# Kernel optimization log

Measured on AMD Instinct MI355X. Metric: run time of the kernel, lower is better.

The kernel has to match this reference:

```python
import jax, jax.numpy as jnp
import numpy as np

WS, SHIFT, NH, DIM = 8, 4, 4, 128
HD = DIM // NH
B, H, W = 16, 128, 128
N = WS * WS
LOG100 = float(np.log(100.0))


def _rel_tables():
    r = np.arange(-(WS - 1), WS, dtype=np.float32)
    tab = np.stack(np.meshgrid(r, r, indexing='ij'), axis=-1) / (WS - 1) * 8.0
    tab = np.sign(tab) * np.log2(np.abs(tab) + 1.0) / np.log2(8.0)
    coords = np.stack(np.meshgrid(np.arange(WS), np.arange(WS), indexing='ij')).reshape(2, -1)
    rel = (coords[:, :, None] - coords[:, None, :]).transpose(1, 2, 0).copy()
    rel[:, :, 0] += WS - 1
    rel[:, :, 1] += WS - 1
    rel[:, :, 0] *= 2 * WS - 1
    return jnp.asarray(tab.reshape(-1, 2)), jnp.asarray(rel.sum(-1))

REL_TABLE, REL_INDEX = _rel_tables()  # ((2WS-1)^2, 2), (N, N)


def _attn_mask():
    img = np.zeros((H, W), np.float32)
    cnt = 0
    for hs in (slice(0, -WS), slice(-WS, -SHIFT), slice(-SHIFT, None)):
        for ws in (slice(0, -WS), slice(-WS, -SHIFT), slice(-SHIFT, None)):
            img[hs, ws] = cnt
            cnt += 1
    mw = img.reshape(H // WS, WS, W // WS, WS).transpose(0, 2, 1, 3).reshape(-1, N)
    d = mw[:, None, :] - mw[:, :, None]
    return jnp.asarray(np.where(d != 0, -100.0, 0.0).astype(np.float32))

ATTN_MASK = _attn_mask()  # (nW, N, N)


def _ln(x, w, b, eps=1e-5):
    mu = x.mean(-1, keepdims=True)
    var = ((x - mu) ** 2).mean(-1, keepdims=True)
    return (x - mu) * jax.lax.rsqrt(var + eps) * w + b


def setup_inputs() -> dict:
    key = jax.random.key(0)
    ks = jax.random.split(key, 8)
    s = 0.02
    return {
        'x': jax.random.normal(ks[0], (B, DIM, H, W), jnp.float32),
        'norm1_w': jnp.ones((DIM,), jnp.float32),
        'norm1_b': jnp.zeros((DIM,), jnp.float32),
        'qkv_w': jax.random.normal(ks[1], (3 * DIM, DIM), jnp.float32) * s,
        'q_bias': jnp.zeros((DIM,), jnp.float32),
        'v_bias': jnp.zeros((DIM,), jnp.float32),
        'logit_scale': jnp.full((NH, 1, 1), float(np.log(10.0)), jnp.float32),
        'cpb_w1': jax.random.normal(ks[2], (512, 2), jnp.float32) * s,
        'cpb_b1': jnp.zeros((512,), jnp.float32),
        'cpb_w2': jax.random.normal(ks[3], (NH, 512), jnp.float32) * s,
        'proj_w': jax.random.normal(ks[4], (DIM, DIM), jnp.float32) * s,
        'proj_b': jnp.zeros((DIM,), jnp.float32),
        'norm2_w': jnp.ones((DIM,), jnp.float32),
        'norm2_b': jnp.zeros((DIM,), jnp.float32),
        'fc1_w': jax.random.normal(ks[5], (4 * DIM, DIM), jnp.float32) * s,
        'fc1_b': jnp.zeros((4 * DIM,), jnp.float32),
        'fc2_w': jax.random.normal(ks[6], (DIM, 4 * DIM), jnp.float32) * s,
        'fc2_b': jnp.zeros((DIM,), jnp.float32),
    }


def reference(x, norm1_w, norm1_b, qkv_w, q_bias, v_bias, logit_scale,
              cpb_w1, cpb_b1, cpb_w2, proj_w, proj_b,
              norm2_w, norm2_b, fc1_w, fc1_b, fc2_w, fc2_b):
    xb = jnp.transpose(x, (0, 2, 3, 1))                 # (B,H,W,C)
    shortcut = xb.reshape(B, H * W, DIM)
    shifted = jnp.roll(xb, (-SHIFT, -SHIFT), axis=(1, 2))
    # window partition -> (B*nW, N, C)
    xw = shifted.reshape(B, H // WS, WS, W // WS, WS, DIM)
    xw = xw.transpose(0, 1, 3, 2, 4, 5).reshape(-1, N, DIM)
    B_ = xw.shape[0]
    qkv_bias = jnp.concatenate([q_bias, jnp.zeros_like(v_bias), v_bias])
    qkv = xw @ qkv_w.T + qkv_bias
    qkv = qkv.reshape(B_, N, 3, NH, HD).transpose(2, 0, 3, 1, 4)
    q, k, v = qkv[0], qkv[1], qkv[2]                    # (B_,NH,N,HD)
    qn = q / jnp.maximum(jnp.linalg.norm(q, axis=-1, keepdims=True), 1e-12)
    kn = k / jnp.maximum(jnp.linalg.norm(k, axis=-1, keepdims=True), 1e-12)
    attn = jnp.einsum('bhnd,bhmd->bhnm', qn, kn)
    attn = attn * jnp.exp(jnp.minimum(logit_scale, LOG100))
    # continuous relative position bias: tiny MLP over log-spaced coords + gather
    tab = jax.nn.relu(REL_TABLE @ cpb_w1.T + cpb_b1) @ cpb_w2.T    # ((2WS-1)^2, NH)
    bias = tab[REL_INDEX.reshape(-1)].reshape(N, N, NH).transpose(2, 0, 1)
    attn = attn + (16.0 * jax.nn.sigmoid(bias))[None]
    nW = ATTN_MASK.shape[0]
    attn = attn.reshape(B_ // nW, nW, NH, N, N) + ATTN_MASK[None, :, None]
    attn = jax.nn.softmax(attn.reshape(B_, NH, N, N), axis=-1)
    out = jnp.einsum('bhnm,bhmd->bhnd', attn, v).transpose(0, 2, 1, 3).reshape(B_, N, DIM)
    out = out @ proj_w.T + proj_b
    # window reverse + reverse cyclic shift
    out = out.reshape(B, H // WS, W // WS, WS, WS, DIM).transpose(0, 1, 3, 2, 4, 5).reshape(B, H, W, DIM)
    out = jnp.roll(out, (SHIFT, SHIFT), axis=(1, 2)).reshape(B, H * W, DIM)
    x1 = shortcut + _ln(out, norm1_w, norm1_b)          # Swin-v2 post-norm residual
    hdn = jax.nn.silu(x1 @ fc1_w.T + fc1_b) @ fc2_w.T + fc2_b
    x2 = x1 + _ln(hdn, norm2_w, norm2_b)
    return x2.reshape(B, H, W, DIM).transpose(0, 3, 1, 2)
```

## Files before the change

kernel.cpp:

```cpp
#include <hip/hip_runtime.h>
#include <cstdint>
#include <cstddef>

typedef __bf16 bf16;
typedef __bf16 bf16x8 __attribute__((ext_vector_type(8)));
typedef float f32x4 __attribute__((ext_vector_type(4)));

#define MFMA16(a, b, c) __builtin_amdgcn_mfma_f32_16x16x32_bf16((a), (b), (c), 0, 0, 0)

__device__ __forceinline__ float bf2f(bf16 v) { return (float)v; }

#define OFF_SCALES 65536
#define OFF_FLAG   65552
#define OFF_QKVB   65600
#define OFF_PROJB  67136
#define OFF_N1W    67648
#define OFF_N1B    68160
#define OFF_FC1B   68672
#define OFF_FC2B   70720
#define OFF_N2W    71232
#define OFF_N2B    71744
#define OFF_QKVW   73728
#define OFF_PROJW  172032
#define OFF_FC1W   204800
#define OFF_FC2W   335872
#define OFF_X1BUF  524288

template<int DT>
__device__ __forceinline__ void g_ld4(const void* base, size_t idx, float* o) {
    if constexpr (DT == 0) {
        uint2 d = *(const uint2*)((const bf16*)base + idx);
        const bf16* p = (const bf16*)&d;
        o[0] = bf2f(p[0]); o[1] = bf2f(p[1]); o[2] = bf2f(p[2]); o[3] = bf2f(p[3]);
    } else {
        float4 d = *(const float4*)((const float*)base + idx);
        o[0] = d.x; o[1] = d.y; o[2] = d.z; o[3] = d.w;
    }
}

__global__ void k_precompute(const void* __restrict__ cpb_w1, const void* __restrict__ cpb_b1,
                             const void* __restrict__ cpb_w2, const void* __restrict__ logit_scale,
                             const void* __restrict__ qkv_w_raw,
                             float* __restrict__ biasAll, float* __restrict__ scales,
                             int* __restrict__ flag)
{
    __shared__ float w1s[1024];
    __shared__ float b1s[512];
    __shared__ float w2s[2048];
    __shared__ float tabv[225][4];
    __shared__ int s_cnt;
    const int t = threadIdx.x;
    if (t == 0) s_cnt = 0;
    __syncthreads();
    {
        const unsigned short* u = (const unsigned short*)qkv_w_raw;
        int c = 0;
        for (int i = t; i < 1024; i += 256) {
            const int e = (u[i] >> 7) & 0xFF;
            if (e >= 0x90 || (e != 0 && e <= 0x60)) ++c;
        }
        atomicAdd(&s_cnt, c);
    }
    __syncthreads();
    const int isf = (s_cnt > 64) ? 1 : 0;
    if (t == 0) *flag = isf;
    if (isf) {
        const float* w1 = (const float*)cpb_w1;
        const float* b1 = (const float*)cpb_b1;
        const float* w2 = (const float*)cpb_w2;
        for (int i = t; i < 1024; i += 256) w1s[i] = w1[i];
        for (int i = t; i < 512;  i += 256) b1s[i] = b1[i];
        for (int i = t; i < 2048; i += 256) w2s[i] = w2[i];
        if (t < 4) scales[t] = expf(fminf(((const float*)logit_scale)[t], 4.6051701859880914f));
    } else {
        const bf16* w1 = (const bf16*)cpb_w1;
        const bf16* b1 = (const bf16*)cpb_b1;
        const bf16* w2 = (const bf16*)cpb_w2;
        for (int i = t; i < 1024; i += 256) w1s[i] = bf2f(w1[i]);
        for (int i = t; i < 512;  i += 256) b1s[i] = bf2f(b1[i]);
        for (int i = t; i < 2048; i += 256) w2s[i] = bf2f(w2[i]);
        if (t < 4) scales[t] = expf(fminf(bf2f(((const bf16*)logit_scale)[t]), 4.6051701859880914f));
    }
    __syncthreads();
    if (t < 225) {
        const int i = t / 15, j = t % 15;
        auto relf = [](int tt) -> float {
            float tf = (float)tt * (8.0f / 7.0f);
            float a = log2f(fabsf(tf) + 1.0f) * (1.0f / 3.0f);
            return tt < 0 ? -a : a;
        };
        const float x0 = relf(i - 7), x1 = relf(j - 7);
        float a0 = 0.f, a1 = 0.f, a2 = 0.f, a3 = 0.f;
        for (int jj = 0; jj < 512; ++jj) {
            float hv = w1s[jj*2] * x0 + w1s[jj*2+1] * x1 + b1s[jj];
            hv = fmaxf(hv, 0.0f);
            a0 += w2s[jj]        * hv;
            a1 += w2s[512 + jj]  * hv;
            a2 += w2s[1024 + jj] * hv;
            a3 += w2s[1536 + jj] * hv;
        }
        tabv[t][0] = a0; tabv[t][1] = a1; tabv[t][2] = a2; tabv[t][3] = a3;
    }
    __syncthreads();
    for (int idx = t; idx < 4*64*64; idx += 256) {
        const int h = idx >> 12, rem = idx & 4095, i = rem >> 6, j = rem & 63;
        const int di = (i >> 3) - (j >> 3) + 7;
        const int dj = (i & 7) - (j & 7) + 7;
        const float bv = tabv[di*15 + dj][h];
        biasAll[idx] = 16.0f / (1.0f + expf(-bv));
    }
}

__global__ void k_convert(
    const void* __restrict__ qkv_w, const void* __restrict__ proj_w,
    const void* __restrict__ fc1w, const void* __restrict__ fc2w,
    const void* __restrict__ q_bias, const void* __restrict__ v_bias,
    const void* __restrict__ proj_b, const void* __restrict__ n1w, const void* __restrict__ n1b,
    const void* __restrict__ fc1b, const void* __restrict__ fc2b,
    const void* __restrict__ n2w, const void* __restrict__ n2b,
    const int* __restrict__ flag, char* __restrict__ ws)
{
    const int isf = *flag;
    const int g  = blockIdx.x * 256 + threadIdx.x;
    const int gs = gridDim.x * 256;
    bf16* qw = (bf16*)(ws + OFF_QKVW);
    bf16* pw = (bf16*)(ws + OFF_PROJW);
    bf16* f1 = (bf16*)(ws + OFF_FC1W);
    bf16* f2 = (bf16*)(ws + OFF_FC2W);
    if (isf) {
        const float* a = (const float*)qkv_w;  for (int i = g; i < 49152; i += gs) qw[i] = (bf16)a[i];
        const float* b = (const float*)proj_w; for (int i = g; i < 16384; i += gs) pw[i] = (bf16)b[i];
        const float* c = (const float*)fc1w;   for (int i = g; i < 65536; i += gs) f1[i] = (bf16)c[i];
        const float* d = (const float*)fc2w;   for (int i = g; i < 65536; i += gs) f2[i] = (bf16)d[i];
    } else {
        const bf16* a = (const bf16*)qkv_w;  for (int i = g; i < 49152; i += gs) qw[i] = a[i];
        const bf16* b = (const bf16*)proj_w; for (int i = g; i < 16384; i += gs) pw[i] = b[i];
        const bf16* c = (const bf16*)fc1w;   for (int i = g; i < 65536; i += gs) f1[i] = c[i];
        const bf16* d = (const bf16*)fc2w;   for (int i = g; i < 65536; i += gs) f2[i] = d[i];
    }
    auto ldf = [&](const void* p, int i) -> float {
        return isf ? ((const float*)p)[i] : bf2f(((const bf16*)p)[i]);
    };
    float* qb  = (float*)(ws + OFF_QKVB);
    float* pb  = (float*)(ws + OFF_PROJB);
    float* w1  = (float*)(ws + OFF_N1W);
    float* b1  = (float*)(ws + OFF_N1B);
    float* f1b = (float*)(ws + OFF_FC1B);
    float* f2b = (float*)(ws + OFF_FC2B);
    float* w2  = (float*)(ws + OFF_N2W);
    float* b2  = (float*)(ws + OFF_N2B);
    for (int i = g; i < 384; i += gs)
        qb[i] = (i < 128) ? ldf(q_bias, i) : ((i < 256) ? 0.0f : ldf(v_bias, i - 256));
    for (int i = g; i < 512; i += gs) f1b[i] = ldf(fc1b, i);
    for (int i = g; i < 128; i += gs) {
        pb[i]  = ldf(proj_b, i); w1[i] = ldf(n1w, i); b1[i] = ldf(n1b, i);
        f2b[i] = ldf(fc2b, i);   w2[i] = ldf(n2w, i); b2[i] = ldf(n2b, i);
    }
}

template<int DT>
__global__ __launch_bounds__(256, 2) void k_attn(
    const void* __restrict__ x,
    const bf16* __restrict__ qkvw, const float* __restrict__ qkvb,
    const bf16* __restrict__ projw, const float* __restrict__ projb,
    const float* __restrict__ n1wf, const float* __restrict__ n1bf,
    const float* __restrict__ biasAll, const float* __restrict__ scales,
    const int* __restrict__ flag, bf16* __restrict__ x1out)
{
    if (*flag != DT) return;

    __shared__ __align__(16) char smem[75008];
    bf16* Xs    = (bf16*)smem;
    bf16* qkvs  = (bf16*)(smem + 17408);
    bf16* Ps    = qkvs;
    bf16* x1s   = qkvs;
    bf16* vs    = (bf16*)(smem + 54272);
    bf16* Os    = vs;
    float* invqs = (float*)(smem + 72704);
    float* invks = (float*)(smem + 73728);
    int*   rid   = (int*)(smem + 74752);

    const int tid  = threadIdx.x;
    const int wv   = tid >> 6;
    const int lane = tid & 63;
    const int l15  = lane & 15;
    const int quad = lane >> 4;

    const int bid = blockIdx.x;
    const int b   = bid >> 8;
    const int wh  = (bid >> 4) & 15;
    const int ww  = bid & 15;

    {
        const int c  = tid & 127;
        const int rb = tid >> 7;
        const int w0 = ww*8 + 4;
        const int w1 = (ww*8 + 8) & 127;
#pragma unroll
        for (int k = 0; k < 4; ++k) {
            const int r    = k*2 + rb;
            const int srch = (wh*8 + r + 4) & 127;
            const size_t rowbase = (((size_t)(b*128 + c))*128 + srch)*128;
            float va[4], vb[4];
            g_ld4<DT>(x, rowbase + w0, va);
            g_ld4<DT>(x, rowbase + w1, vb);
#pragma unroll
            for (int j = 0; j < 4; ++j) {
                Xs[(r*8 + j)*136 + c]     = (bf16)va[j];
                Xs[(r*8 + 4 + j)*136 + c] = (bf16)vb[j];
            }
        }
        if (tid < 64) {
            const int rr = tid >> 3, cc = tid & 7;
            const int hs = wh*8 + rr, wsc = ww*8 + cc;
            const int rh = (hs  < 120) ? 0 : ((hs  < 124) ? 1 : 2);
            const int rw = (wsc < 120) ? 0 : ((wsc < 124) ? 1 : 2);
            rid[tid] = rh*3 + rw;
        }
    }
    __syncthreads();

    {
        f32x4 acc[4][6];
#pragma unroll
        for (int mt = 0; mt < 4; ++mt)
#pragma unroll
            for (int nl = 0; nl < 6; ++nl) acc[mt][nl] = (f32x4){0.f, 0.f, 0.f, 0.f};
#pragma unroll
        for (int ks = 0; ks < 4; ++ks) {
            bf16x8 a[4];
#pragma unroll
            for (int mt = 0; mt < 4; ++mt)
                a[mt] = *(const bf16x8*)&Xs[(mt*16 + l15)*136 + ks*32 + quad*8];
#pragma unroll
            for (int nl = 0; nl < 6; ++nl) {
                const int o = (wv*6 + nl)*16 + l15;
                bf16x8 bw = *(const bf16x8*)&qkvw[(size_t)o*128 + ks*32 + quad*8];
#pragma unroll
                for (int mt = 0; mt < 4; ++mt)
                    acc[mt][nl] = MFMA16(a[mt], bw, acc[mt][nl]);
            }
        }
#pragma unroll
        for (int nl = 0; nl < 6; ++nl) {
            const int col = (wv*6 + nl)*16 + l15;
            const float bias = qkvb[col];
#pragma unroll
            for (int mt = 0; mt < 4; ++mt)
#pragma unroll
                for (int r = 0; r < 4; ++r) {
                    const int row = mt*16 + quad*4 + r;
                    const float v = acc[mt][nl][r] + bias;
                    if (col < 256) qkvs[row*264 + col] = (bf16)v;
                    else           vs[(col - 256)*72 + row] = (bf16)v;
                }
        }
    }
    __syncthreads();

    {
        const int n = lane;
        const bf16* qrow = &qkvs[n*264 + wv*32];
        const bf16* krow = &qkvs[n*264 + 128 + wv*32];
        float sq = 0.f, sk = 0.f;
#pragma unroll
        for (int dd = 0; dd < 4; ++dd) {
            bf16x8 vq = *(const bf16x8*)(qrow + dd*8);
            bf16x8 vk = *(const bf16x8*)(krow + dd*8);
#pragma unroll
            for (int e = 0; e < 8; ++e) {
                const float fq = (float)vq[e]; sq += fq*fq;
                const float fk = (float)vk[e]; sk += fk*fk;
            }
        }
        invqs[wv*64 + n] = 1.0f / fmaxf(sqrtf(sq), 1e-12f);
        invks[wv*64 + n] = 1.0f / fmaxf(sqrtf(sk), 1e-12f);
    }
    __syncthreads();

    {
        const float scale = scales[wv];
        f32x4 s[4][4];
#pragma unroll
        for (int mt = 0; mt < 4; ++mt)
#pragma unroll
            for (int nt = 0; nt < 4; ++nt) s[mt][nt] = (f32x4){0.f, 0.f, 0.f, 0.f};
        bf16x8 aq[4];
#pragma unroll
        for (int mt = 0; mt < 4; ++mt)
            aq[mt] = *(const bf16x8*)&qkvs[(mt*16 + l15)*264 + wv*32 + quad*8];
#pragma unroll
        for (int nt = 0; nt < 4; ++nt) {
            bf16x8 bk = *(const bf16x8*)&qkvs[(nt*16 + l15)*264 + 128 + wv*32 + quad*8];
#pragma unroll
            for (int mt = 0; mt < 4; ++mt)
                s[mt][nt] = MFMA16(aq[mt], bk, s[mt][nt]);
        }
        __syncthreads();
        const float* bg = biasAll + wv*4096;
        const bool bnd = (wh == 15) || (ww == 15);
        float ikj[4]; int rj[4];
#pragma unroll
        for (int nt = 0; nt < 4; ++nt) {
            ikj[nt] = invks[wv*64 + nt*16 + l15];
            rj[nt]  = rid[nt*16 + l15];
        }
#pragma unroll
        for (int mt = 0; mt < 4; ++mt)
#pragma unroll
            for (int r = 0; r < 4; ++r) {
                const int i = mt*16 + quad*4 + r;
                const float iqs = invqs[wv*64 + i] * scale;
                const int ri = rid[i];
#pragma unroll
                for (int nt = 0; nt < 4; ++nt) {
                    const int j = nt*16 + l15;
                    float v = s[mt][nt][r] * (iqs * ikj[nt]) + bg[i*64 + j];
                    if (bnd && (ri != rj[nt])) v -= 100.0f;
                    s[mt][nt][r] = v;
                }
            }
#pragma unroll
        for (int mt = 0; mt < 4; ++mt) {
            float mx[4], sm[4];
#pragma unroll
            for (int r = 0; r < 4; ++r) {
                float m = fmaxf(fmaxf(s[mt][0][r], s[mt][1][r]), fmaxf(s[mt][2][r], s[mt][3][r]));
                m = fmaxf(m, __shfl_xor(m, 1));
                m = fmaxf(m, __shfl_xor(m, 2));
                m = fmaxf(m, __shfl_xor(m, 4));
                m = fmaxf(m, __shfl_xor(m, 8));
                mx[r] = m; sm[r] = 0.f;
            }
#pragma unroll
            for (int nt = 0; nt < 4; ++nt)
#pragma unroll
                for (int r = 0; r < 4; ++r) {
                    const float e = __expf(s[mt][nt][r] - mx[r]);
                    s[mt][nt][r] = e;
                    sm[r] += e;
                }
#pragma unroll
            for (int r = 0; r < 4; ++r) {
                float t2 = sm[r];
                t2 += __shfl_xor(t2, 1);
                t2 += __shfl_xor(t2, 2);
                t2 += __shfl_xor(t2, 4);
                t2 += __shfl_xor(t2, 8);
                sm[r] = 1.0f / t2;
            }
#pragma unroll
            for (int nt = 0; nt < 4; ++nt)
#pragma unroll
                for (int r = 0; r < 4; ++r) {
                    const float p = s[mt][nt][r] * sm[r];
                    Ps[wv*64*72 + (mt*16 + quad*4 + r)*72 + nt*16 + l15] = (bf16)p;
                }
        }
    }
    __syncthreads();

    {
        f32x4 o[4][2];
#pragma unroll
        for (int mt = 0; mt < 4; ++mt)
#pragma unroll
            for (int nt = 0; nt < 2; ++nt) o[mt][nt] = (f32x4){0.f, 0.f, 0.f, 0.f};
#pragma unroll
        for (int ks = 0; ks < 2; ++ks) {
            bf16x8 ap[4];
#pragma unroll
            for (int mt = 0; mt < 4; ++mt)
                ap[mt] = *(const bf16x8*)&Ps[wv*64*72 + (mt*16 + l15)*72 + ks*32 + quad*8];
#pragma unroll
            for (int nt = 0; nt < 2; ++nt) {
                bf16x8 bv = *(const bf16x8*)&vs[(wv*32 + nt*16 + l15)*72 + ks*32 + quad*8];
#pragma unroll
                for (int mt = 0; mt < 4; ++mt)
                    o[mt][nt] = MFMA16(ap[mt], bv, o[mt][nt]);
            }
        }
        __syncthreads();
#pragma unroll
        for (int mt = 0; mt < 4; ++mt)
#pragma unroll
            for (int nt = 0; nt < 2; ++nt)
#pragma unroll
                for (int r = 0; r < 4; ++r) {
                    const int i = mt*16 + quad*4 + r;
                    Os[i*136 + wv*32 + nt*16 + l15] = (bf16)o[mt][nt][r];
                }
    }
    __syncthreads();

    {
        f32x4 pa[4][2];
#pragma unroll
        for (int mt = 0; mt < 4; ++mt)
#pragma unroll
            for (int nt = 0; nt < 2; ++nt) pa[mt][nt] = (f32x4){0.f, 0.f, 0.f, 0.f};
#pragma unroll
        for (int ks = 0; ks < 4; ++ks) {
            bf16x8 ao[4];
#pragma unroll
            for (int mt = 0; mt < 4; ++mt)
                ao[mt] = *(const bf16x8*)&Os[(mt*16 + l15)*136 + ks*32 + quad*8];
#pragma unroll
            for (int nt = 0; nt < 2; ++nt) {
                const int oc = wv*32 + nt*16 + l15;
                bf16x8 bw = *(const bf16x8*)&projw[(size_t)oc*128 + ks*32 + quad*8];
#pragma unroll
                for (int mt = 0; mt < 4; ++mt)
                    pa[mt][nt] = MFMA16(ao[mt], bw, pa[mt][nt]);
            }
        }
        float pb[2], wn[2], bn[2];
#pragma unroll
        for (int nt = 0; nt < 2; ++nt) {
            const int oc = wv*32 + nt*16 + l15;
            pb[nt] = projb[oc]; wn[nt] = n1wf[oc]; bn[nt] = n1bf[oc];
        }
        float* ps = invqs;
        float* pq = invks;
#pragma unroll
        for (int mt = 0; mt < 4; ++mt)
#pragma unroll
            for (int r = 0; r < 4; ++r) {
                pa[mt][0][r] += pb[0];
                pa[mt][1][r] += pb[1];
                float sv = pa[mt][0][r] + pa[mt][1][r];
                sv += __shfl_xor(sv, 1); sv += __shfl_xor(sv, 2);
                sv += __shfl_xor(sv, 4); sv += __shfl_xor(sv, 8);
                if (l15 == 0) ps[wv*64 + mt*16 + quad*4 + r] = sv;
            }
        __syncthreads();
        float mu[4][4];
#pragma unroll
        for (int mt = 0; mt < 4; ++mt)
#pragma unroll
            for (int r = 0; r < 4; ++r) {
                const int i = mt*16 + quad*4 + r;
                mu[mt][r] = (ps[i] + ps[64+i] + ps[128+i] + ps[192+i]) * (1.0f/128.0f);
                const float d0 = pa[mt][0][r] - mu[mt][r];
                const float d1 = pa[mt][1][r] - mu[mt][r];
                float sv = d0*d0 + d1*d1;
                sv += __shfl_xor(sv, 1); sv += __shfl_xor(sv, 2);
                sv += __shfl_xor(sv, 4); sv += __shfl_xor(sv, 8);
                if (l15 == 0) pq[wv*64 + i] = sv;
            }
        __syncthreads();
#pragma unroll
        for (int mt = 0; mt < 4; ++mt)
#pragma unroll
            for (int r = 0; r < 4; ++r) {
                const int i = mt*16 + quad*4 + r;
                const float var = (pq[i] + pq[64+i] + pq[128+i] + pq[192+i]) * (1.0f/128.0f);
                const float rstd = rsqrtf(var + 1e-5f);
#pragma unroll
                for (int nt = 0; nt < 2; ++nt) {
                    const int oc = wv*32 + nt*16 + l15;
                    const float y = (pa[mt][nt][r] - mu[mt][r]) * rstd * wn[nt] + bn[nt];
                    const float x1v = bf2f(Xs[i*136 + oc]) + y;
                    x1s[i*136 + oc] = (bf16)x1v;
                }
            }
    }
    __syncthreads();

    {
        const int n = tid >> 2, part = tid & 3;
        const int rr = n >> 3, cc = n & 7;
        const int hf = (wh*8 + rr + 4) & 127;
        const int wf = (ww*8 + cc + 4) & 127;
        bf16* dst = x1out + ((size_t)b*16384 + hf*128 + wf)*128 + part*32;
        const uint4* srcq = (const uint4*)&x1s[n*136 + part*32];
#pragma unroll
        for (int k2 = 0; k2 < 4; ++k2)
            ((uint4*)dst)[k2] = srcq[k2];
    }
}

template<int DT>
__global__ __launch_bounds__(256, 4) void k_mlp(
    const bf16* __restrict__ x1, const bf16* __restrict__ fc1w, const float* __restrict__ fc1bf,
    const bf16* __restrict__ fc2w, const float* __restrict__ fc2bf,
    const float* __restrict__ n2wf, const float* __restrict__ n2bf,
    const int* __restrict__ flag, void* __restrict__ out)
{
    if (*flag != DT) return;

    __shared__ __align__(16) bf16 x1s[64*136];
    __shared__ __align__(16) bf16 hs[64*136];
    __shared__ float ps[256];
    __shared__ float pq[256];

    const int tid  = threadIdx.x;
    const int wv   = tid >> 6;
    const int lane = tid & 63;
    const int l15  = lane & 15;
    const int quad = lane >> 4;
    const int bid  = blockIdx.x;

    {
        const int n = tid >> 2, part = tid & 3;
        const uint4* src = (const uint4*)(x1 + ((size_t)bid*64 + n)*128 + part*32);
        uint4* dst = (uint4*)&x1s[n*136 + part*32];
#pragma unroll
        for (int k = 0; k < 4; ++k) dst[k] = src[k];
    }
    __syncthreads();

    f32x4 ya[4][2];
#pragma unroll
    for (int mt = 0; mt < 4; ++mt)
#pragma unroll
        for (int nt = 0; nt < 2; ++nt) ya[mt][nt] = (f32x4){0.f, 0.f, 0.f, 0.f};

#pragma unroll
    for (int ch = 0; ch < 4; ++ch) {
        if (ch) __syncthreads();
        f32x4 ha[4][2];
#pragma unroll
        for (int mt = 0; mt < 4; ++mt)
#pragma unroll
            for (int nt = 0; nt < 2; ++nt) ha[mt][nt] = (f32x4){0.f, 0.f, 0.f, 0.f};
#pragma unroll
        for (int ks = 0; ks < 4; ++ks) {
            bf16x8 a[4];
#pragma unroll
            for (int mt = 0; mt < 4; ++mt)
                a[mt] = *(const bf16x8*)&x1s[(mt*16 + l15)*136 + ks*32 + quad*8];
#pragma unroll
            for (int nt = 0; nt < 2; ++nt) {
                const int hid = ch*128 + wv*32 + nt*16 + l15;
                bf16x8 bw = *(const bf16x8*)&fc1w[(size_t)hid*128 + ks*32 + quad*8];
#pragma unroll
                for (int mt = 0; mt < 4; ++mt)
                    ha[mt][nt] = MFMA16(a[mt], bw, ha[mt][nt]);
            }
        }
#pragma unroll
        for (int nt = 0; nt < 2; ++nt) {
            const int hid = ch*128 + wv*32 + nt*16 + l15;
            const float bb = fc1bf[hid];
            const int hl = wv*32 + nt*16 + l15;
#pragma unroll
            for (int mt = 0; mt < 4; ++mt)
#pragma unroll
                for (int r = 0; r < 4; ++r) {
                    float v = ha[mt][nt][r] + bb;
                    v = v / (1.0f + __expf(-v));
                    hs[(mt*16 + quad*4 + r)*136 + hl] = (bf16)v;
                }
        }
        __syncthreads();
#pragma unroll
        for (int ks = 0; ks < 4; ++ks) {
            bf16x8 ah[4];
#pragma unroll
            for (int mt = 0; mt < 4; ++mt)
                ah[mt] = *(const bf16x8*)&hs[(mt*16 + l15)*136 + ks*32 + quad*8];
#pragma unroll
            for (int nt = 0; nt < 2; ++nt) {
                const int oc = wv*32 + nt*16 + l15;
                bf16x8 bw = *(const bf16x8*)&fc2w[(size_t)oc*512 + ch*128 + ks*32 + quad*8];
#pragma unroll
                for (int mt = 0; mt < 4; ++mt)
                    ya[mt][nt] = MFMA16(ah[mt], bw, ya[mt][nt]);
            }
        }
    }
    __syncthreads();

    {
        float pb[2], wn[2], bn[2];
#pragma unroll
        for (int nt = 0; nt < 2; ++nt) {
            const int oc = wv*32 + nt*16 + l15;
            pb[nt] = fc2bf[oc]; wn[nt] = n2wf[oc]; bn[nt] = n2bf[oc];
        }
#pragma unroll
        for (int mt = 0; mt < 4; ++mt)
#pragma unroll
            for (int r = 0; r < 4; ++r) {
                ya[mt][0][r] += pb[0];
                ya[mt][1][r] += pb[1];
                float sv = ya[mt][0][r] + ya[mt][1][r];
                sv += __shfl_xor(sv, 1); sv += __shfl_xor(sv, 2);
                sv += __shfl_xor(sv, 4); sv += __shfl_xor(sv, 8);
                if (l15 == 0) ps[wv*64 + mt*16 + quad*4 + r] = sv;
            }
        __syncthreads();
        float mu[4][4];
#pragma unroll
        for (int mt = 0; mt < 4; ++mt)
#pragma unroll
            for (int r = 0; r < 4; ++r) {
                const int i = mt*16 + quad*4 + r;
                mu[mt][r] = (ps[i] + ps[64+i] + ps[128+i] + ps[192+i]) * (1.0f/128.0f);
                const float d0 = ya[mt][0][r] - mu[mt][r];
                const float d1 = ya[mt][1][r] - mu[mt][r];
                float sv = d0*d0 + d1*d1;
                sv += __shfl_xor(sv, 1); sv += __shfl_xor(sv, 2);
                sv += __shfl_xor(sv, 4); sv += __shfl_xor(sv, 8);
                if (l15 == 0) pq[wv*64 + i] = sv;
            }
        __syncthreads();
        bf16* x2s = hs;
#pragma unroll
        for (int mt = 0; mt < 4; ++mt)
#pragma unroll
            for (int r = 0; r < 4; ++r) {
                const int i = mt*16 + quad*4 + r;
                const float var = (pq[i] + pq[64+i] + pq[128+i] + pq[192+i]) * (1.0f/128.0f);
                const float rstd = rsqrtf(var + 1e-5f);
#pragma unroll
                for (int nt = 0; nt < 2; ++nt) {
                    const int oc = wv*32 + nt*16 + l15;
                    const float yv = (ya[mt][nt][r] - mu[mt][r]) * rstd * wn[nt] + bn[nt];
                    const float x2v = bf2f(x1s[i*136 + oc]) + yv;
                    x2s[i*136 + oc] = (bf16)x2v;
                }
            }
    }
    __syncthreads();

    {
        const int c = tid >> 1, half = tid & 1;
        const int b = bid >> 8, rem = bid & 255;
        const int hh = rem >> 1, w0 = (rem & 1)*64;
        const bf16* x2s = hs;
        const size_t base_off = ((size_t)(b*128 + c))*16384 + hh*128 + w0 + half*32;
        if constexpr (DT == 0) {
            const unsigned short* x2u = (const unsigned short*)hs;
            bf16* dst = (bf16*)out + base_off;
#pragma unroll
            for (int g = 0; g < 4; ++g) {
                const int tb = half*32 + g*8;
                uint4 u;
                u.x = (unsigned)x2u[(tb+0)*136 + c] | ((unsigned)x2u[(tb+1)*136 + c] << 16);
                u.y = (unsigned)x2u[(tb+2)*136 + c] | ((unsigned)x2u[(tb+3)*136 + c] << 16);
                u.z = (unsigned)x2u[(tb+4)*136 + c] | ((unsigned)x2u[(tb+5)*136 + c] << 16);
                u.w = (unsigned)x2u[(tb+6)*136 + c] | ((unsigned)x2u[(tb+7)*136 + c] << 16);
                ((uint4*)dst)[g] = u;
            }
        } else {
            float* dst = (float*)out + base_off;
#pragma unroll
            for (int g = 0; g < 4; ++g) {
                const int tb = half*32 + g*8;
                float4 u0, u1;
                u0.x = bf2f(x2s[(tb+0)*136 + c]); u0.y = bf2f(x2s[(tb+1)*136 + c]);
                u0.z = bf2f(x2s[(tb+2)*136 + c]); u0.w = bf2f(x2s[(tb+3)*136 + c]);
                u1.x = bf2f(x2s[(tb+4)*136 + c]); u1.y = bf2f(x2s[(tb+5)*136 + c]);
                u1.z = bf2f(x2s[(tb+6)*136 + c]); u1.w = bf2f(x2s[(tb+7)*136 + c]);
                ((float4*)dst)[2*g]     = u0;
                ((float4*)dst)[2*g + 1] = u1;
            }
        }
    }
}

extern "C" void kernel_launch(void* const* d_in, const int* in_sizes, int n_in,
                              void* d_out, int out_size, void* d_ws, size_t ws_size,
                              hipStream_t stream)
{
    (void)in_sizes; (void)n_in; (void)out_size; (void)ws_size;
    const void* x      = d_in[0];
    const void* n1w    = d_in[1];
    const void* n1b    = d_in[2];
    const void* qkv_w  = d_in[3];
    const void* q_bias = d_in[4];
    const void* v_bias = d_in[5];
    const void* lscale = d_in[6];
    const void* cpb_w1 = d_in[7];
    const void* cpb_b1 = d_in[8];
    const void* cpb_w2 = d_in[9];
    const void* proj_w = d_in[10];
    const void* proj_b = d_in[11];
    const void* n2w    = d_in[12];
    const void* n2b    = d_in[13];
    const void* fc1w   = d_in[14];
    const void* fc1b   = d_in[15];
    const void* fc2w   = d_in[16];
    const void* fc2b   = d_in[17];

    char*  ws      = (char*)d_ws;
    float* biasAll = (float*)ws;
    float* scales  = (float*)(ws + OFF_SCALES);
    int*   flag    = (int*)(ws + OFF_FLAG);
    bf16*  x1buf   = (bf16*)(ws + OFF_X1BUF);

    k_precompute<<<dim3(1), dim3(256), 0, stream>>>(cpb_w1, cpb_b1, cpb_w2, lscale, qkv_w,
                                                    biasAll, scales, flag);
    k_convert<<<dim3(96), dim3(256), 0, stream>>>(qkv_w, proj_w, fc1w, fc2w,
                                                  q_bias, v_bias, proj_b, n1w, n1b,
                                                  fc1b, fc2b, n2w, n2b, flag, ws);
    k_attn<0><<<dim3(4096), dim3(256), 0, stream>>>(x,
        (const bf16*)(ws + OFF_QKVW), (const float*)(ws + OFF_QKVB),
        (const bf16*)(ws + OFF_PROJW), (const float*)(ws + OFF_PROJB),
        (const float*)(ws + OFF_N1W), (const float*)(ws + OFF_N1B),
        biasAll, scales, flag, x1buf);
    k_attn<1><<<dim3(4096), dim3(256), 0, stream>>>(x,
        (const bf16*)(ws + OFF_QKVW), (const float*)(ws + OFF_QKVB),
        (const bf16*)(ws + OFF_PROJW), (const float*)(ws + OFF_PROJB),
        (const float*)(ws + OFF_N1W), (const float*)(ws + OFF_N1B),
        biasAll, scales, flag, x1buf);
    k_mlp<0><<<dim3(4096), dim3(256), 0, stream>>>(x1buf,
        (const bf16*)(ws + OFF_FC1W), (const float*)(ws + OFF_FC1B),
        (const bf16*)(ws + OFF_FC2W), (const float*)(ws + OFF_FC2B),
        (const float*)(ws + OFF_N2W), (const float*)(ws + OFF_N2B), flag, d_out);
    k_mlp<1><<<dim3(4096), dim3(256), 0, stream>>>(x1buf,
        (const bf16*)(ws + OFF_FC1W), (const float*)(ws + OFF_FC1B),
        (const bf16*)(ws + OFF_FC2W), (const float*)(ws + OFF_FC2B),
        (const float*)(ws + OFF_N2W), (const float*)(ws + OFF_N2B), flag, d_out);
}
```

Baseline: 717.3 us.

## Fuse attention and MLP into one per-window kernel, dropping x1 buffer

Merges the attention/projection/LN kernel with the MLP/LN kernel so each window block keeps x1 in shared memory and runs fc1, SiLU, fc2 and the second LayerNorm before writing the output directly in NCHW with the reverse shift. This removes the global write and read of the intermediate x1 tensor and one kernel launch. It also remaps block indices so consecutive blocks span different batches/windows. In exchange the MLP now runs at the attention kernel's occupancy and the final stores become short scattered row segments instead of long contiguous ones.

```diff
diff --git a/kernel.cpp b/kernel.cpp
--- a/kernel.cpp
+++ b/kernel.cpp
@@ -24,7 +24,6 @@
 #define OFF_PROJW  172032
 #define OFF_FC1W   204800
 #define OFF_FC2W   335872
-#define OFF_X1BUF  524288
 
 template<int DT>
 __device__ __forceinline__ void g_ld4(const void* base, size_t idx, float* o) {
@@ -159,13 +158,16 @@
 }
 
 template<int DT>
-__global__ __launch_bounds__(256, 2) void k_attn(
+__global__ __launch_bounds__(256, 2) void k_fused(
     const void* __restrict__ x,
     const bf16* __restrict__ qkvw, const float* __restrict__ qkvb,
     const bf16* __restrict__ projw, const float* __restrict__ projb,
     const float* __restrict__ n1wf, const float* __restrict__ n1bf,
+    const bf16* __restrict__ fc1w, const float* __restrict__ fc1bf,
+    const bf16* __restrict__ fc2w, const float* __restrict__ fc2bf,
+    const float* __restrict__ n2wf, const float* __restrict__ n2bf,
     const float* __restrict__ biasAll, const float* __restrict__ scales,
-    const int* __restrict__ flag, bf16* __restrict__ x1out)
+    const int* __restrict__ flag, void* __restrict__ out)
 {
     if (*flag != DT) return;
 
@@ -176,9 +178,12 @@
     bf16* x1s   = qkvs;
     bf16* vs    = (bf16*)(smem + 54272);
     bf16* Os    = vs;
+    bf16* hs    = vs;
     float* invqs = (float*)(smem + 72704);
     float* invks = (float*)(smem + 73728);
     int*   rid   = (int*)(smem + 74752);
+    float* psum = invqs;
+    float* pvar = invks;
 
     const int tid  = threadIdx.x;
     const int wv   = tid >> 6;
@@ -186,7 +191,8 @@
     const int l15  = lane & 15;
     const int quad = lane >> 4;
 
-    const int bid = blockIdx.x;
+    const int bid0 = blockIdx.x;
+    const int bid  = ((bid0 & 7) << 9) | (bid0 >> 3);
     const int b   = bid >> 8;
     const int wh  = (bid >> 4) & 15;
     const int ww  = bid & 15;
@@ -212,8 +218,8 @@
         }
         if (tid < 64) {
             const int rr = tid >> 3, cc = tid & 7;
-            const int hs = wh*8 + rr, wsc = ww*8 + cc;
-            const int rh = (hs  < 120) ? 0 : ((hs  < 124) ? 1 : 2);
+            const int hs_ = wh*8 + rr, wsc = ww*8 + cc;
+            const int rh = (hs_ < 120) ? 0 : ((hs_ < 124) ? 1 : 2);
             const int rw = (wsc < 120) ? 0 : ((wsc < 124) ? 1 : 2);
             rid[tid] = rh*3 + rw;
         }
@@ -420,8 +426,6 @@
             const int oc = wv*32 + nt*16 + l15;
             pb[nt] = projb[oc]; wn[nt] = n1wf[oc]; bn[nt] = n1bf[oc];
         }
-        float* ps = invqs;
-        float* pq = invks;
 #pragma unroll
         for (int mt = 0; mt < 4; ++mt)
 #pragma unroll
@@ -431,7 +435,7 @@
                 float sv = pa[mt][0][r] + pa[mt][1][r];
                 sv += __shfl_xor(sv, 1); sv += __shfl_xor(sv, 2);
                 sv += __shfl_xor(sv, 4); sv += __shfl_xor(sv, 8);
-                if (l15 == 0) ps[wv*64 + mt*16 + quad*4 + r] = sv;
+                if (l15 == 0) psum[wv*64 + mt*16 + quad*4 + r] = sv;
             }
         __syncthreads();
         float mu[4][4];
@@ -440,13 +444,13 @@
 #pragma unroll
             for (int r = 0; r < 4; ++r) {
                 const int i = mt*16 + quad*4 + r;
-                mu[mt][r] = (ps[i] + ps[64+i] + ps[128+i] + ps[192+i]) * (1.0f/128.0f);
+                mu[mt][r] = (psum[i] + psum[64+i] + psum[128+i] + psum[192+i]) * (1.0f/128.0f);
                 const float d0 = pa[mt][0][r] - mu[mt][r];
                 const float d1 = pa[mt][1][r] - mu[mt][r];
                 float sv = d0*d0 + d1*d1;
                 sv += __shfl_xor(sv, 1); sv += __shfl_xor(sv, 2);
                 sv += __shfl_xor(sv, 4); sv += __shfl_xor(sv, 8);
-                if (l15 == 0) pq[wv*64 + i] = sv;
+                if (l15 == 0) pvar[wv*64 + i] = sv;
             }
         __syncthreads();
 #pragma unroll
@@ -454,7 +458,7 @@
 #pragma unroll
             for (int r = 0; r < 4; ++r) {
                 const int i = mt*16 + quad*4 + r;
-                const float var = (pq[i] + pq[64+i] + pq[128+i] + pq[192+i]) * (1.0f/128.0f);
+                const float var = (pvar[i] + pvar[64+i] + pvar[128+i] + pvar[192+i]) * (1.0f/128.0f);
                 const float rstd = rsqrtf(var + 1e-5f);
 #pragma unroll
                 for (int nt = 0; nt < 2; ++nt) {
@@ -467,49 +471,6 @@
     }
     __syncthreads();
 
-    {
-        const int n = tid >> 2, part = tid & 3;
-        const int rr = n >> 3, cc = n & 7;
-        const int hf = (wh*8 + rr + 4) & 127;
-        const int wf = (ww*8 + cc + 4) & 127;
-        bf16* dst = x1out + ((size_t)b*16384 + hf*128 + wf)*128 + part*32;
-        const uint4* srcq = (const uint4*)&x1s[n*136 + part*32];
-#pragma unroll
-        for (int k2 = 0; k2 < 4; ++k2)
-            ((uint4*)dst)[k2] = srcq[k2];
-    }
-}
-
-template<int DT>
-__global__ __launch_bounds__(256, 4) void k_mlp(
-    const bf16* __restrict__ x1, const bf16* __restrict__ fc1w, const float* __restrict__ fc1bf,
-    const bf16* __restrict__ fc2w, const float* __restrict__ fc2bf,
-    const float* __restrict__ n2wf, const float* __restrict__ n2bf,
-    const int* __restrict__ flag, void* __restrict__ out)
-{
-    if (*flag != DT) return;
-
-    __shared__ __align__(16) bf16 x1s[64*136];
-    __shared__ __align__(16) bf16 hs[64*136];
-    __shared__ float ps[256];
-    __shared__ float pq[256];
-
-    const int tid  = threadIdx.x;
-    const int wv   = tid >> 6;
-    const int lane = tid & 63;
-    const int l15  = lane & 15;
-    const int quad = lane >> 4;
-    const int bid  = blockIdx.x;
-
-    {
-        const int n = tid >> 2, part = tid & 3;
-        const uint4* src = (const uint4*)(x1 + ((size_t)bid*64 + n)*128 + part*32);
-        uint4* dst = (uint4*)&x1s[n*136 + part*32];
-#pragma unroll
-        for (int k = 0; k < 4; ++k) dst[k] = src[k];
-    }
-    __syncthreads();
-
     f32x4 ya[4][2];
 #pragma unroll
     for (int mt = 0; mt < 4; ++mt)
@@ -588,7 +549,7 @@
                 float sv = ya[mt][0][r] + ya[mt][1][r];
                 sv += __shfl_xor(sv, 1); sv += __shfl_xor(sv, 2);
                 sv += __shfl_xor(sv, 4); sv += __shfl_xor(sv, 8);
-                if (l15 == 0) ps[wv*64 + mt*16 + quad*4 + r] = sv;
+                if (l15 == 0) psum[wv*64 + mt*16 + quad*4 + r] = sv;
             }
         __syncthreads();
         float mu[4][4];
@@ -597,13 +558,13 @@
 #pragma unroll
             for (int r = 0; r < 4; ++r) {
                 const int i = mt*16 + quad*4 + r;
-                mu[mt][r] = (ps[i] + ps[64+i] + ps[128+i] + ps[192+i]) * (1.0f/128.0f);
+                mu[mt][r] = (psum[i] + psum[64+i] + psum[128+i] + psum[192+i]) * (1.0f/128.0f);
                 const float d0 = ya[mt][0][r] - mu[mt][r];
                 const float d1 = ya[mt][1][r] - mu[mt][r];
                 float sv = d0*d0 + d1*d1;
                 sv += __shfl_xor(sv, 1); sv += __shfl_xor(sv, 2);
                 sv += __shfl_xor(sv, 4); sv += __shfl_xor(sv, 8);
-                if (l15 == 0) pq[wv*64 + i] = sv;
+                if (l15 == 0) pvar[wv*64 + i] = sv;
             }
         __syncthreads();
         bf16* x2s = hs;
@@ -612,7 +573,7 @@
 #pragma unroll
             for (int r = 0; r < 4; ++r) {
                 const int i = mt*16 + quad*4 + r;
-                const float var = (pq[i] + pq[64+i] + pq[128+i] + pq[192+i]) * (1.0f/128.0f);
+                const float var = (pvar[i] + pvar[64+i] + pvar[128+i] + pvar[192+i]) * (1.0f/128.0f);
                 const float rstd = rsqrtf(var + 1e-5f);
 #pragma unroll
                 for (int nt = 0; nt < 2; ++nt) {
@@ -626,36 +587,35 @@
     __syncthreads();
 
     {
-        const int c = tid >> 1, half = tid & 1;
-        const int b = bid >> 8, rem = bid & 255;
-        const int hh = rem >> 1, w0 = (rem & 1)*64;
         const bf16* x2s = hs;
-        const size_t base_off = ((size_t)(b*128 + c))*16384 + hh*128 + w0 + half*32;
-        if constexpr (DT == 0) {
-            const unsigned short* x2u = (const unsigned short*)hs;
-            bf16* dst = (bf16*)out + base_off;
-#pragma unroll
-            for (int g = 0; g < 4; ++g) {
-                const int tb = half*32 + g*8;
-                uint4 u;
-                u.x = (unsigned)x2u[(tb+0)*136 + c] | ((unsigned)x2u[(tb+1)*136 + c] << 16);
-                u.y = (unsigned)x2u[(tb+2)*136 + c] | ((unsigned)x2u[(tb+3)*136 + c] << 16);
-                u.z = (unsigned)x2u[(tb+4)*136 + c] | ((unsigned)x2u[(tb+5)*136 + c] << 16);
-                u.w = (unsigned)x2u[(tb+6)*136 + c] | ((unsigned)x2u[(tb+7)*136 + c] << 16);
-                ((uint4*)dst)[g] = u;
-            }
-        } else {
-            float* dst = (float*)out + base_off;
-#pragma unroll
-            for (int g = 0; g < 4; ++g) {
-                const int tb = half*32 + g*8;
+        const int wf0 = ww*8 + 4;
+        const int wf1 = (ww*8 + 8) & 127;
+#pragma unroll
+        for (int g = 0; g < 4; ++g) {
+            const int idx = g*256 + tid;
+            const int c  = idx & 127;
+            const int rr = idx >> 7;
+            const int hf = (wh*8 + rr + 4) & 127;
+            const size_t rowb = ((size_t)(b*128 + c))*16384 + (size_t)hf*128;
+            if constexpr (DT == 0) {
+                const unsigned short* xu = (const unsigned short*)x2s;
+                uint2 u0, u1;
+                u0.x = (unsigned)xu[(rr*8+0)*136 + c] | ((unsigned)xu[(rr*8+1)*136 + c] << 16);
+                u0.y = (unsigned)xu[(rr*8+2)*136 + c] | ((unsigned)xu[(rr*8+3)*136 + c] << 16);
+                u1.x = (unsigned)xu[(rr*8+4)*136 + c] | ((unsigned)xu[(rr*8+5)*136 + c] << 16);
+                u1.y = (unsigned)xu[(rr*8+6)*136 + c] | ((unsigned)xu[(rr*8+7)*136 + c] << 16);
+                bf16* dstb = (bf16*)out;
+                *(uint2*)(dstb + rowb + wf0) = u0;
+                *(uint2*)(dstb + rowb + wf1) = u1;
+            } else {
                 float4 u0, u1;
-                u0.x = bf2f(x2s[(tb+0)*136 + c]); u0.y = bf2f(x2s[(tb+1)*136 + c]);
-                u0.z = bf2f(x2s[(tb+2)*136 + c]); u0.w = bf2f(x2s[(tb+3)*136 + c]);
-                u1.x = bf2f(x2s[(tb+4)*136 + c]); u1.y = bf2f(x2s[(tb+5)*136 + c]);
-                u1.z = bf2f(x2s[(tb+6)*136 + c]); u1.w = bf2f(x2s[(tb+7)*136 + c]);
-                ((float4*)dst)[2*g]     = u0;
-                ((float4*)dst)[2*g + 1] = u1;
+                u0.x = bf2f(x2s[(rr*8+0)*136 + c]); u0.y = bf2f(x2s[(rr*8+1)*136 + c]);
+                u0.z = bf2f(x2s[(rr*8+2)*136 + c]); u0.w = bf2f(x2s[(rr*8+3)*136 + c]);
+                u1.x = bf2f(x2s[(rr*8+4)*136 + c]); u1.y = bf2f(x2s[(rr*8+5)*136 + c]);
+                u1.z = bf2f(x2s[(rr*8+6)*136 + c]); u1.w = bf2f(x2s[(rr*8+7)*136 + c]);
+                float* dstf = (float*)out;
+                *(float4*)(dstf + rowb + wf0) = u0;
+                *(float4*)(dstf + rowb + wf1) = u1;
             }
         }
     }
@@ -689,29 +649,26 @@
     float* biasAll = (float*)ws;
     float* scales  = (float*)(ws + OFF_SCALES);
     int*   flag    = (int*)(ws + OFF_FLAG);
-    bf16*  x1buf   = (bf16*)(ws + OFF_X1BUF);
 
     k_precompute<<<dim3(1), dim3(256), 0, stream>>>(cpb_w1, cpb_b1, cpb_w2, lscale, qkv_w,
                                                     biasAll, scales, flag);
     k_convert<<<dim3(96), dim3(256), 0, stream>>>(qkv_w, proj_w, fc1w, fc2w,
                                                   q_bias, v_bias, proj_b, n1w, n1b,
                                                   fc1b, fc2b, n2w, n2b, flag, ws);
-    k_attn<0><<<dim3(4096), dim3(256), 0, stream>>>(x,
+    k_fused<0><<<dim3(4096), dim3(256), 0, stream>>>(x,
         (const bf16*)(ws + OFF_QKVW), (const float*)(ws + OFF_QKVB),
         (const bf16*)(ws + OFF_PROJW), (const float*)(ws + OFF_PROJB),
         (const float*)(ws + OFF_N1W), (const float*)(ws + OFF_N1B),
-        biasAll, scales, flag, x1buf);
-    k_attn<1><<<dim3(4096), dim3(256), 0, stream>>>(x,
+        (const bf16*)(ws + OFF_FC1W), (const float*)(ws + OFF_FC1B),
+        (const bf16*)(ws + OFF_FC2W), (const float*)(ws + OFF_FC2B),
+        (const float*)(ws + OFF_N2W), (const float*)(ws + OFF_N2B),
+        biasAll, scales, flag, d_out);
+    k_fused<1><<<dim3(4096), dim3(256), 0, stream>>>(x,
         (const bf16*)(ws + OFF_QKVW), (const float*)(ws + OFF_QKVB),
         (const bf16*)(ws + OFF_PROJW), (const float*)(ws + OFF_PROJB),
         (const float*)(ws + OFF_N1W), (const float*)(ws + OFF_N1B),
-        biasAll, scales, flag, x1buf);
-    k_mlp<0><<<dim3(4096), dim3(256), 0, stream>>>(x1buf,
         (const bf16*)(ws + OFF_FC1W), (const float*)(ws + OFF_FC1B),
         (const bf16*)(ws + OFF_FC2W), (const float*)(ws + OFF_FC2B),
-        (const float*)(ws + OFF_N2W), (const float*)(ws + OFF_N2B), flag, d_out);
-    k_mlp<1><<<dim3(4096), dim3(256), 0, stream>>>(x1buf,
-        (const bf16*)(ws + OFF_FC1W), (const float*)(ws + OFF_FC1B),
-        (const bf16*)(ws + OFF_FC2W), (const float*)(ws + OFF_FC2B),
-        (const float*)(ws + OFF_N2W), (const float*)(ws + OFF_N2B), flag, d_out);
+        (const float*)(ws + OFF_N2W), (const float*)(ws + OFF_N2B),
+        biasAll, scales, flag, d_out);
 }
```

Result: faster. 701.4 us (-2.2%).
